# Kernel tuning notes

Measured on AMD Instinct MI355X. Metric: run time of the kernel, lower is better.

The kernel has to match this reference:

```python
import jax, jax.numpy as jnp
import numpy as np

B, N = 2, 2048
TOP_K = 48
NUM_RBF = 16
MAX_REL = 32            # max_relative_feature
NUM_POS = 16            # num_positional_embeddings
EDGE_FEATURES = 128
EDGE_IN = NUM_POS + NUM_RBF * 25  # 416
POS_IN = 2 * MAX_REL + 2          # 66 one-hot classes


def setup_inputs() -> dict:
    key = jax.random.key(0)
    k0, k1, k2, k3 = jax.random.split(key, 4)
    X = jax.random.normal(k0, (B, N, 4, 3), dtype=jnp.float32) * 3.0
    mask = jnp.ones((B, N), dtype=jnp.float32)
    R_idx = jnp.arange(B * N, dtype=jnp.int32).reshape(B, N)
    chain_labels = jax.random.randint(k1, (B, N), 0, 4).astype(jnp.int32)
    W_pos = 0.05 * jax.random.normal(k2, (POS_IN, NUM_POS), dtype=jnp.float32)
    b_pos = jnp.zeros((NUM_POS,), dtype=jnp.float32)
    W_edge = 0.05 * jax.random.normal(k3, (EDGE_IN, EDGE_FEATURES), dtype=jnp.float32)
    b_edge = jnp.zeros((EDGE_FEATURES,), dtype=jnp.float32)
    return {"X": X, "mask": mask, "R_idx": R_idx, "chain_labels": chain_labels,
            "W_pos": W_pos, "b_pos": b_pos, "W_edge": W_edge, "b_edge": b_edge}


def _rbf(D):
    # D: [..., K] -> [..., K, NUM_RBF]
    mu = jnp.linspace(2.0, 22.0, NUM_RBF)        # D_min=2, D_max=22
    sigma = (22.0 - 2.0) / NUM_RBF               # 1.25
    return jnp.exp(-(((D[..., None] - mu) / sigma) ** 2))


def _pair_dist(A, Bc):
    # A, Bc: [B, N, 3] -> [B, N, N]
    return jnp.sqrt(jnp.sum((A[:, :, None, :] - Bc[:, None, :, :]) ** 2, axis=-1) + 1e-6)


def reference(X, mask, R_idx, chain_labels, W_pos, b_pos, W_edge, b_edge):
    # virtual Cbeta from backbone geometry
    b = X[:, :, 1, :] - X[:, :, 0, :]
    c = X[:, :, 2, :] - X[:, :, 1, :]
    a = jnp.cross(b, c, axis=-1)
    Cb = -0.58273431 * a + 0.56802827 * b - 0.54067466 * c + X[:, :, 1, :]
    Ca, Nat, Cat, Oat = X[:, :, 1, :], X[:, :, 0, :], X[:, :, 2, :], X[:, :, 3, :]

    # masked Ca-Ca distances + k nearest neighbors
    mask2 = mask[:, None, :] * mask[:, :, None]
    D = mask2 * _pair_dist(Ca, Ca)
    D_adjust = D + (1.0 - mask2) * jnp.max(D, axis=-1, keepdims=True)
    neg_D, E_idx = jax.lax.top_k(-D_adjust, min(TOP_K, N))  # smallest distances
    D_neighbors = -neg_D                                     # [B, N, K]

    rbfs = [_rbf(D_neighbors)]
    pairs = [(Nat, Nat), (Cat, Cat), (Oat, Oat), (Cb, Cb),
             (Ca, Nat), (Ca, Cat), (Ca, Oat), (Ca, Cb),
             (Nat, Cat), (Nat, Oat), (Nat, Cb), (Cb, Cat), (Cb, Oat), (Oat, Cat),
             (Nat, Ca), (Cat, Ca), (Oat, Ca), (Cb, Ca),
             (Cat, Nat), (Oat, Nat), (Cb, Nat), (Cat, Cb), (Oat, Cb), (Cat, Oat)]
    for A_, B_ in pairs:  # fixed structural set of 24 atom-pair types
        Dab = _pair_dist(A_, B_)                          # [B, N, N]
        Dn = jnp.take_along_axis(Dab, E_idx, axis=2)      # [B, N, K]
        rbfs.append(_rbf(Dn))
    RBF_all = jnp.concatenate(rbfs, axis=-1)              # [B, N, K, 25*NUM_RBF]

    # relative positional / chain features at the gathered neighbors
    offset = R_idx[:, :, None] - R_idx[:, None, :]
    offset = jnp.take_along_axis(offset, E_idx, axis=2)   # [B, N, K]
    d_chains = (chain_labels[:, :, None] == chain_labels[:, None, :]).astype(jnp.int32)
    E_chains = jnp.take_along_axis(d_chains, E_idx, axis=2)

    d = jnp.clip(offset + MAX_REL, 0, 2 * MAX_REL)
    d = d * E_chains + (1 - E_chains) * (2 * MAX_REL + 1)
    d_onehot = jax.nn.one_hot(d, POS_IN, dtype=jnp.float32)  # [B, N, K, 66]
    E_positional = d_onehot @ W_pos + b_pos                  # [B, N, K, 16]

    E = jnp.concatenate((E_positional, RBF_all), axis=-1)    # [B, N, K, 416]
    E = E @ W_edge + b_edge                                  # [B, N, K, 128]
    return E, E_idx
```

## Files before the change

### kernel.cpp

```cpp
#include <hip/hip_runtime.h>
#include <hip/hip_bf16.h>
#include <stdint.h>

#define BB   2
#define NN   2048
#define BN   (BB*NN)
#define KTOP 48
#define EIN  416
#define EF   128
#define LROW 424

typedef __attribute__((ext_vector_type(8))) short s8v;
typedef __attribute__((ext_vector_type(4))) float f32x4;
typedef unsigned short u16;
typedef unsigned int u32;
typedef unsigned long long u64;

__device__ __constant__ int cPA[25] = {1,0,2,3,4,1,1,1,1,0,0,0,4,4,3,0,2,3,4,2,3,4,2,3,2};
__device__ __constant__ int cPB[25] = {1,0,2,3,4,0,2,3,4,2,3,4,2,3,2,1,1,1,1,0,0,0,4,4,3};

__device__ __forceinline__ u16 bf16u(float x) {
  __hip_bfloat16 h = __float2bfloat16(x);
  return *reinterpret_cast<u16*>(&h);
}

__global__ __launch_bounds__(256) void prep_kernel(const float* __restrict__ X,
                                                   const float* __restrict__ W_edge,
                                                   float* __restrict__ atoms5,
                                                   float* __restrict__ capack,
                                                   u16* __restrict__ wt) {
  int tid = blockIdx.x * 256 + threadIdx.x;
  if (tid < EIN * EF) {
    int n = tid & (EF - 1), kk = tid >> 7;
    wt[(size_t)n * EIN + kk] = bf16u(W_edge[tid]);
  } else if (tid < EIN * EF + BN) {
    int idx = tid - EIN * EF;
    const float* x = X + (size_t)idx * 12;
    float Nx = x[0], Ny = x[1], Nz = x[2];
    float Cax = x[3], Cay = x[4], Caz = x[5];
    float Cx = x[6], Cy = x[7], Cz = x[8];
    float Ox = x[9], Oy = x[10], Oz = x[11];
    float bx = Cax - Nx, by = Cay - Ny, bz = Caz - Nz;
    float cx = Cx - Cax, cy = Cy - Cay, cz = Cz - Caz;
    float ax = by * cz - bz * cy;
    float ay = bz * cx - bx * cz;
    float az = bx * cy - by * cx;
    float Cbx = -0.58273431f * ax + 0.56802827f * bx - 0.54067466f * cx + Cax;
    float Cby = -0.58273431f * ay + 0.56802827f * by - 0.54067466f * cy + Cay;
    float Cbz = -0.58273431f * az + 0.56802827f * bz - 0.54067466f * cz + Caz;
    float* o = atoms5 + (size_t)idx * 15;
    o[0] = Nx;  o[1] = Ny;  o[2] = Nz;
    o[3] = Cax; o[4] = Cay; o[5] = Caz;
    o[6] = Cx;  o[7] = Cy;  o[8] = Cz;
    o[9] = Ox;  o[10] = Oy; o[11] = Oz;
    o[12] = Cbx; o[13] = Cby; o[14] = Cbz;
    capack[idx * 3 + 0] = Cax;
    capack[idx * 3 + 1] = Cay;
    capack[idx * 3 + 2] = Caz;
  }
}

__device__ __forceinline__ u32 blockExclScan(u32 v, u32* scanw, int t) {
  int lane = t & 63, w = t >> 6;
  u32 inc = v;
#pragma unroll
  for (int off = 1; off < 64; off <<= 1) {
    u32 o = __shfl_up(inc, off);
    if (lane >= off) inc += o;
  }
  if (lane == 63) scanw[w] = inc;
  __syncthreads();
  u32 base = 0;
  for (int ww = 0; ww < w; ++ww) base += scanw[ww];
  __syncthreads();
  return base + inc - v;
}

template<int NB, bool CHKPREF>
__device__ __forceinline__ void radix_round(u32* hist, u32* scanw, u32* selinfo, int t,
                                            const u32* kv, u32 pref, int prefShift,
                                            int binShift, u32 binMask, u32 r) {
  const int PB = NB / 256;
  for (int q = 0; q < PB; ++q) hist[t * PB + q] = 0;
  __syncthreads();
#pragma unroll
  for (int s = 0; s < 8; ++s) {
    bool ok = (!CHKPREF) || ((kv[s] >> prefShift) == pref);
    if (ok) atomicAdd(&hist[(kv[s] >> binShift) & binMask], 1u);
  }
  __syncthreads();
  u32 loc[PB];
  u32 sum = 0;
  for (int q = 0; q < PB; ++q) { loc[q] = hist[t * PB + q]; sum += loc[q]; }
  int lane = t & 63, w = t >> 6;
  u32 inc = sum;
#pragma unroll
  for (int off = 1; off < 64; off <<= 1) {
    u32 o = __shfl_up(inc, off);
    if (lane >= off) inc += o;
  }
  if (lane == 63) scanw[w] = inc;
  __syncthreads();
  u32 base = 0;
  for (int ww = 0; ww < w; ++ww) base += scanw[ww];
  u32 c = base + inc - sum;
  for (int q = 0; q < PB; ++q) {
    u32 nc = c + loc[q];
    if (c < r && r <= nc) { selinfo[0] = (u32)(t * PB + q); selinfo[1] = r - c; }
    c = nc;
  }
  __syncthreads();
}

__global__ __launch_bounds__(256) void topk_kernel(const float* __restrict__ capack,
                                                   const float* __restrict__ mask,
                                                   int* __restrict__ eidx,
                                                   float* __restrict__ dtop,
                                                   float* __restrict__ eidx_f) {
  __shared__ u32 hist[4096];
  __shared__ u32 scanw[4];
  __shared__ u32 selinfo[2];
  __shared__ float redf[4];
  __shared__ u64 win[64];

  int row = blockIdx.x;
  int b = row >> 11, i = row & (NN - 1);
  int t = threadIdx.x, lane = t & 63, w = t >> 6;
  const float* cab = capack + (size_t)b * NN * 3;
  const float* mrow = mask + (size_t)b * NN;
  float cix = cab[i * 3 + 0], ciy = cab[i * 3 + 1], ciz = cab[i * 3 + 2];
  float mi = mrow[i];

  float dvv[8], m2v[8];
  float lmax = 0.f;
#pragma unroll
  for (int s = 0; s < 8; ++s) {
    int j = t * 8 + s;
    float dx = cix - cab[j * 3 + 0];
    float dy = ciy - cab[j * 3 + 1];
    float dz = ciz - cab[j * 3 + 2];
    float d = sqrtf(dx * dx + dy * dy + dz * dz + 1e-6f);
    float m2 = mi * mrow[j];
    float D = m2 * d;
    dvv[s] = D; m2v[s] = m2;
    lmax = fmaxf(lmax, D);
  }
#pragma unroll
  for (int off = 32; off >= 1; off >>= 1) lmax = fmaxf(lmax, __shfl_xor(lmax, off));
  if (lane == 0) redf[w] = lmax;
  __syncthreads();
  float rmax = fmaxf(fmaxf(redf[0], redf[1]), fmaxf(redf[2], redf[3]));

  u32 kv[8];
#pragma unroll
  for (int s = 0; s < 8; ++s)
    kv[s] = __float_as_uint(dvv[s] + (1.0f - m2v[s]) * rmax);

  u32 r = KTOP;
  radix_round<4096, false>(hist, scanw, selinfo, t, kv, 0, 0, 20, 0xFFFu, r);
  u32 sel1 = selinfo[0]; r = selinfo[1];
  radix_round<1024, true>(hist, scanw, selinfo, t, kv, sel1, 20, 10, 0x3FFu, r);
  u32 sel2 = selinfo[0]; r = selinfo[1];
  u32 pref12 = (sel1 << 10) | sel2;
  radix_round<1024, true>(hist, scanw, selinfo, t, kv, pref12, 10, 0, 0x3FFu, r);
  u32 sel3 = selinfo[0];
  u32 takeEq = selinfo[1];
  u32 T = (sel1 << 20) | (sel2 << 10) | sel3;

  u32 lcnt = 0, ecnt = 0;
#pragma unroll
  for (int s = 0; s < 8; ++s) { lcnt += (kv[s] < T); ecnt += (kv[s] == T); }
  u32 ebase = blockExclScan(ecnt, scanw, t);
  u32 taken = 0;
  if (ebase < takeEq) { u32 room = takeEq - ebase; taken = room < ecnt ? room : ecnt; }
  u32 wbase = blockExclScan(lcnt + taken, scanw, t);
  u32 slot = wbase, tleft = taken;
#pragma unroll
  for (int s = 0; s < 8; ++s) {
    u32 j = (u32)(t * 8 + s);
    if (kv[s] < T) {
      win[slot++] = ((u64)kv[s] << 32) | j;
    } else if (kv[s] == T && tleft) {
      win[slot++] = ((u64)kv[s] << 32) | j;
      tleft--;
    }
  }
  __syncthreads();

  if (w == 0) {
    u64 key = (lane < KTOP) ? win[lane] : ~0ull;
#pragma unroll
    for (int k = 2; k <= 64; k <<= 1) {
#pragma unroll
      for (int jj = k >> 1; jj >= 1; jj >>= 1) {
        u64 p = __shfl_xor(key, jj);
        bool lowerl = (lane & jj) == 0;
        bool asc = (lane & k) == 0;
        u64 mn = p < key ? p : key;
        u64 mx = p < key ? key : p;
        key = (lowerl == asc) ? mn : mx;
      }
    }
    if (lane < KTOP) {
      u32 j = (u32)(key & 0xffffffffu);
      eidx[row * KTOP + lane] = (int)j;
      eidx_f[row * KTOP + lane] = (float)j;
      dtop[row * KTOP + lane] = __uint_as_float((u32)(key >> 32));
    }
  }
}

__global__ __launch_bounds__(256) void edge_kernel(const float* __restrict__ atoms5,
                                                   const u16* __restrict__ wt,
                                                   const int* __restrict__ eidx,
                                                   const float* __restrict__ dtop,
                                                   const int* __restrict__ Ridx,
                                                   const int* __restrict__ chains,
                                                   const float* __restrict__ Wpos,
                                                   const float* __restrict__ bpos,
                                                   const float* __restrict__ bedge,
                                                   float* __restrict__ Eout) {
  __shared__ u16 feat[KTOP * LROW];
  __shared__ float atomsJ[KTOP][15];
  __shared__ float atomsI[15];
  __shared__ int jbuf[KTOP];

  int row = blockIdx.x;
  int b = row >> 11, i = row & (NN - 1);
  int t = threadIdx.x;

  if (t < KTOP) jbuf[t] = eidx[row * KTOP + t];
  if (t < 15) atomsI[t] = atoms5[(size_t)row * 15 + t];
  __syncthreads();

  if (t < KTOP * 5) {
    int k = t / 5, a = t % 5;
    int j = jbuf[k];
    const float* src = atoms5 + ((size_t)(b * NN + j) * 15 + a * 3);
    atomsJ[k][a * 3 + 0] = src[0];
    atomsJ[k][a * 3 + 1] = src[1];
    atomsJ[k][a * 3 + 2] = src[2];
  }
  __syncthreads();

  if (t < KTOP) {
    int k = t, j = jbuf[k];
    int Ri = Ridx[b * NN + i], Rj = Ridx[b * NN + j];
    int same = (chains[b * NN + i] == chains[b * NN + j]);
    int off = Ri - Rj + 32;
    off = off < 0 ? 0 : (off > 64 ? 64 : off);
    int drow = same ? off : 65;
#pragma unroll
    for (int r = 0; r < 16; ++r)
      feat[k * LROW + r] = bf16u(Wpos[drow * 16 + r] + bpos[r]);
    float D = dtop[row * KTOP + k];
#pragma unroll
    for (int r = 0; r < 16; ++r) {
      float mu = 2.0f + (20.0f * r) / 15.0f;
      float tt = (D - mu) * 0.8f;
      feat[k * LROW + 16 + r] = bf16u(__expf(-tt * tt));
    }
  }
  if (t < KTOP * 5) {
    int k = t / 5, g = t % 5;
    for (int p = 1 + g; p < 25; p += 5) {
      int a = cPA[p], b2 = cPB[p];
      float dx = atomsI[a * 3 + 0] - atomsJ[k][b2 * 3 + 0];
      float dy = atomsI[a * 3 + 1] - atomsJ[k][b2 * 3 + 1];
      float dz = atomsI[a * 3 + 2] - atomsJ[k][b2 * 3 + 2];
      float D = sqrtf(dx * dx + dy * dy + dz * dz + 1e-6f);
#pragma unroll
      for (int r = 0; r < 16; ++r) {
        float mu = 2.0f + (20.0f * r) / 15.0f;
        float tt = (D - mu) * 0.8f;
        feat[k * LROW + 16 + p * 16 + r] = bf16u(__expf(-tt * tt));
      }
    }
  }
  __syncthreads();

  int w = t >> 6, lane = t & 63;
  int lr = lane & 15, lg = lane >> 4;
  f32x4 acc[3][2] = {};
  for (int kc = 0; kc < 13; ++kc) {
    s8v afrag[3];
#pragma unroll
    for (int mt = 0; mt < 3; ++mt)
      afrag[mt] = *reinterpret_cast<const s8v*>(&feat[(mt * 16 + lr) * LROW + kc * 32 + lg * 8]);
#pragma unroll
    for (int nt = 0; nt < 2; ++nt) {
      int col = w * 32 + nt * 16 + lr;
      s8v bfrag = *reinterpret_cast<const s8v*>(&wt[(size_t)col * EIN + kc * 32 + lg * 8]);
#pragma unroll
      for (int mt = 0; mt < 3; ++mt)
        acc[mt][nt] = __builtin_amdgcn_mfma_f32_16x16x32_bf16(afrag[mt], bfrag, acc[mt][nt], 0, 0, 0);
    }
  }
#pragma unroll
  for (int nt = 0; nt < 2; ++nt) {
    int col = w * 32 + nt * 16 + lr;
    float bias = bedge[col];
#pragma unroll
    for (int mt = 0; mt < 3; ++mt) {
#pragma unroll
      for (int q = 0; q < 4; ++q) {
        int m = mt * 16 + lg * 4 + q;
        Eout[((size_t)row * KTOP + m) * EF + col] = acc[mt][nt][q] + bias;
      }
    }
  }
}

extern "C" void kernel_launch(void* const* d_in, const int* in_sizes, int n_in,
                              void* d_out, int out_size, void* d_ws, size_t ws_size,
                              hipStream_t stream) {
  const float* X = (const float*)d_in[0];
  const float* mask = (const float*)d_in[1];
  const int* Ridx = (const int*)d_in[2];
  const int* chains = (const int*)d_in[3];
  const float* Wpos = (const float*)d_in[4];
  const float* bpos = (const float*)d_in[5];
  const float* Wedge = (const float*)d_in[6];
  const float* bedge = (const float*)d_in[7];

  float* Eout = (float*)d_out;
  float* EidxF = Eout + (size_t)BN * KTOP * EF;

  float* atoms5 = (float*)d_ws;
  float* capack = atoms5 + (size_t)BN * 15;
  u16* wt = (u16*)(capack + (size_t)BN * 3);
  int* eidx = (int*)(wt + (size_t)EIN * EF);
  float* dtop = (float*)(eidx + (size_t)BN * KTOP);

  int prep_threads = EIN * EF + BN;
  prep_kernel<<<(prep_threads + 255) / 256, 256, 0, stream>>>(X, Wedge, atoms5, capack, wt);
  topk_kernel<<<BN, 256, 0, stream>>>(capack, mask, eidx, dtop, EidxF);
  edge_kernel<<<BN, 256, 0, stream>>>(atoms5, wt, eidx, dtop, Ridx, chains, Wpos, bpos, bedge, Eout);
}
```

Measured before the change: 100.3 us.

## Vectorize loads, reformulate RBF recurrence, stage output stores through LDS

Pads atom and Ca coordinates to float4 so gathers become single vector loads, and re-lays out the bf16 weight matrix so MFMA B-fragment loads are contiguous across columns. The edge kernel now builds features with one thread per (neighbor, 16-wide feature chunk), computes the 16 RBF values with a multiplicative recurrence (two exps instead of sixteen) and writes them as packed 16-byte stores. The GEMM output is staged in LDS and written as coalesced float4 rows, and the histogram clear/read in the top-k radix is vectorised. Distances are clamped to 40 for the recurrence, which changes rounding slightly, and an extra barrier is added for the staging step.

```diff
diff --git a/kernel.cpp b/kernel.cpp
--- a/kernel.cpp
+++ b/kernel.cpp
@@ -9,9 +9,11 @@
 #define EIN  416
 #define EF   128
 #define LROW 424
+#define SROW 132
 
 typedef __attribute__((ext_vector_type(8))) short s8v;
 typedef __attribute__((ext_vector_type(4))) float f32x4;
+typedef __attribute__((ext_vector_type(4))) unsigned int u32x4;
 typedef unsigned short u16;
 typedef unsigned int u32;
 typedef unsigned long long u64;
@@ -23,16 +25,19 @@
   __hip_bfloat16 h = __float2bfloat16(x);
   return *reinterpret_cast<u16*>(&h);
 }
+__device__ __forceinline__ u32 pack2(float lo, float hi) {
+  return (u32)bf16u(lo) | ((u32)bf16u(hi) << 16);
+}
 
 __global__ __launch_bounds__(256) void prep_kernel(const float* __restrict__ X,
                                                    const float* __restrict__ W_edge,
-                                                   float* __restrict__ atoms5,
-                                                   float* __restrict__ capack,
-                                                   u16* __restrict__ wt) {
+                                                   float* __restrict__ atoms5p,
+                                                   float* __restrict__ capack4,
+                                                   u16* __restrict__ wtf) {
   int tid = blockIdx.x * 256 + threadIdx.x;
   if (tid < EIN * EF) {
-    int n = tid & (EF - 1), kk = tid >> 7;
-    wt[(size_t)n * EIN + kk] = bf16u(W_edge[tid]);
+    int k = tid >> 7, n = tid & 127;
+    wtf[((size_t)(k >> 3)) * 1024 + n * 8 + (k & 7)] = bf16u(W_edge[tid]);
   } else if (tid < EIN * EF + BN) {
     int idx = tid - EIN * EF;
     const float* x = X + (size_t)idx * 12;
@@ -48,15 +53,13 @@
     float Cbx = -0.58273431f * ax + 0.56802827f * bx - 0.54067466f * cx + Cax;
     float Cby = -0.58273431f * ay + 0.56802827f * by - 0.54067466f * cy + Cay;
     float Cbz = -0.58273431f * az + 0.56802827f * bz - 0.54067466f * cz + Caz;
-    float* o = atoms5 + (size_t)idx * 15;
-    o[0] = Nx;  o[1] = Ny;  o[2] = Nz;
-    o[3] = Cax; o[4] = Cay; o[5] = Caz;
-    o[6] = Cx;  o[7] = Cy;  o[8] = Cz;
-    o[9] = Ox;  o[10] = Oy; o[11] = Oz;
-    o[12] = Cbx; o[13] = Cby; o[14] = Cbz;
-    capack[idx * 3 + 0] = Cax;
-    capack[idx * 3 + 1] = Cay;
-    capack[idx * 3 + 2] = Caz;
+    f32x4* o = (f32x4*)(atoms5p + (size_t)idx * 20);
+    o[0] = (f32x4){Nx, Ny, Nz, 0.f};
+    o[1] = (f32x4){Cax, Cay, Caz, 0.f};
+    o[2] = (f32x4){Cx, Cy, Cz, 0.f};
+    o[3] = (f32x4){Ox, Oy, Oz, 0.f};
+    o[4] = (f32x4){Cbx, Cby, Cbz, 0.f};
+    *(f32x4*)(capack4 + (size_t)idx * 4) = (f32x4){Cax, Cay, Caz, 0.f};
   }
 }
 
@@ -81,7 +84,9 @@
                                             const u32* kv, u32 pref, int prefShift,
                                             int binShift, u32 binMask, u32 r) {
   const int PB = NB / 256;
-  for (int q = 0; q < PB; ++q) hist[t * PB + q] = 0;
+#pragma unroll
+  for (int q = 0; q < PB / 4; ++q)
+    *(u32x4*)&hist[t * PB + q * 4] = (u32x4){0, 0, 0, 0};
   __syncthreads();
 #pragma unroll
   for (int s = 0; s < 8; ++s) {
@@ -91,7 +96,13 @@
   __syncthreads();
   u32 loc[PB];
   u32 sum = 0;
-  for (int q = 0; q < PB; ++q) { loc[q] = hist[t * PB + q]; sum += loc[q]; }
+#pragma unroll
+  for (int q = 0; q < PB / 4; ++q) {
+    u32x4 lv = *(u32x4*)&hist[t * PB + q * 4];
+    loc[q * 4 + 0] = lv.x; loc[q * 4 + 1] = lv.y;
+    loc[q * 4 + 2] = lv.z; loc[q * 4 + 3] = lv.w;
+    sum += lv.x + lv.y + lv.z + lv.w;
+  }
   int lane = t & 63, w = t >> 6;
   u32 inc = sum;
 #pragma unroll
@@ -104,6 +115,7 @@
   u32 base = 0;
   for (int ww = 0; ww < w; ++ww) base += scanw[ww];
   u32 c = base + inc - sum;
+#pragma unroll
   for (int q = 0; q < PB; ++q) {
     u32 nc = c + loc[q];
     if (c < r && r <= nc) { selinfo[0] = (u32)(t * PB + q); selinfo[1] = r - c; }
@@ -112,9 +124,8 @@
   __syncthreads();
 }
 
-__global__ __launch_bounds__(256) void topk_kernel(const float* __restrict__ capack,
+__global__ __launch_bounds__(256) void topk_kernel(const float* __restrict__ capack4,
                                                    const float* __restrict__ mask,
-                                                   int* __restrict__ eidx,
                                                    float* __restrict__ dtop,
                                                    float* __restrict__ eidx_f) {
   __shared__ u32 hist[4096];
@@ -126,21 +137,22 @@
   int row = blockIdx.x;
   int b = row >> 11, i = row & (NN - 1);
   int t = threadIdx.x, lane = t & 63, w = t >> 6;
-  const float* cab = capack + (size_t)b * NN * 3;
+  const float* cab4 = capack4 + (size_t)b * NN * 4;
   const float* mrow = mask + (size_t)b * NN;
-  float cix = cab[i * 3 + 0], ciy = cab[i * 3 + 1], ciz = cab[i * 3 + 2];
+  f32x4 ci = *(const f32x4*)&cab4[(size_t)i * 4];
   float mi = mrow[i];
+  f32x4 mk0 = *(const f32x4*)&mrow[t * 8];
+  f32x4 mk1 = *(const f32x4*)&mrow[t * 8 + 4];
 
   float dvv[8], m2v[8];
   float lmax = 0.f;
 #pragma unroll
   for (int s = 0; s < 8; ++s) {
-    int j = t * 8 + s;
-    float dx = cix - cab[j * 3 + 0];
-    float dy = ciy - cab[j * 3 + 1];
-    float dz = ciz - cab[j * 3 + 2];
+    f32x4 cj = *(const f32x4*)&cab4[(size_t)(t * 8 + s) * 4];
+    float dx = ci.x - cj.x, dy = ci.y - cj.y, dz = ci.z - cj.z;
     float d = sqrtf(dx * dx + dy * dy + dz * dz + 1e-6f);
-    float m2 = mi * mrow[j];
+    float mj = (s < 4) ? mk0[s] : mk1[s - 4];
+    float m2 = mi * mj;
     float D = m2 * d;
     dvv[s] = D; m2v[s] = m2;
     lmax = fmaxf(lmax, D);
@@ -203,78 +215,81 @@
     }
     if (lane < KTOP) {
       u32 j = (u32)(key & 0xffffffffu);
-      eidx[row * KTOP + lane] = (int)j;
       eidx_f[row * KTOP + lane] = (float)j;
       dtop[row * KTOP + lane] = __uint_as_float((u32)(key >> 32));
     }
   }
 }
 
-__global__ __launch_bounds__(256) void edge_kernel(const float* __restrict__ atoms5,
-                                                   const u16* __restrict__ wt,
-                                                   const int* __restrict__ eidx,
-                                                   const float* __restrict__ dtop,
-                                                   const int* __restrict__ Ridx,
-                                                   const int* __restrict__ chains,
-                                                   const float* __restrict__ Wpos,
-                                                   const float* __restrict__ bpos,
-                                                   const float* __restrict__ bedge,
-                                                   float* __restrict__ Eout) {
-  __shared__ u16 feat[KTOP * LROW];
-  __shared__ float atomsJ[KTOP][15];
-  __shared__ float atomsI[15];
+__global__ __launch_bounds__(256, 4) void edge_kernel(const float* __restrict__ atoms5p,
+                                                      const u16* __restrict__ wtf,
+                                                      const float* __restrict__ eidx_f,
+                                                      const float* __restrict__ dtop,
+                                                      const int* __restrict__ Ridx,
+                                                      const int* __restrict__ chains,
+                                                      const float* __restrict__ Wpos,
+                                                      const float* __restrict__ bpos,
+                                                      const float* __restrict__ bedge,
+                                                      float* __restrict__ Eout) {
+  __shared__ __align__(16) u16 featsm[KTOP * LROW];
   __shared__ int jbuf[KTOP];
 
   int row = blockIdx.x;
   int b = row >> 11, i = row & (NN - 1);
   int t = threadIdx.x;
 
-  if (t < KTOP) jbuf[t] = eidx[row * KTOP + t];
-  if (t < 15) atomsI[t] = atoms5[(size_t)row * 15 + t];
-  __syncthreads();
-
-  if (t < KTOP * 5) {
-    int k = t / 5, a = t % 5;
-    int j = jbuf[k];
-    const float* src = atoms5 + ((size_t)(b * NN + j) * 15 + a * 3);
-    atomsJ[k][a * 3 + 0] = src[0];
-    atomsJ[k][a * 3 + 1] = src[1];
-    atomsJ[k][a * 3 + 2] = src[2];
-  }
-  __syncthreads();
-
-  if (t < KTOP) {
-    int k = t, j = jbuf[k];
-    int Ri = Ridx[b * NN + i], Rj = Ridx[b * NN + j];
-    int same = (chains[b * NN + i] == chains[b * NN + j]);
-    int off = Ri - Rj + 32;
-    off = off < 0 ? 0 : (off > 64 ? 64 : off);
-    int drow = same ? off : 65;
-#pragma unroll
-    for (int r = 0; r < 16; ++r)
-      feat[k * LROW + r] = bf16u(Wpos[drow * 16 + r] + bpos[r]);
-    float D = dtop[row * KTOP + k];
-#pragma unroll
-    for (int r = 0; r < 16; ++r) {
-      float mu = 2.0f + (20.0f * r) / 15.0f;
-      float tt = (D - mu) * 0.8f;
-      feat[k * LROW + 16 + r] = bf16u(__expf(-tt * tt));
-    }
-  }
-  if (t < KTOP * 5) {
-    int k = t / 5, g = t % 5;
-    for (int p = 1 + g; p < 25; p += 5) {
-      int a = cPA[p], b2 = cPB[p];
-      float dx = atomsI[a * 3 + 0] - atomsJ[k][b2 * 3 + 0];
-      float dy = atomsI[a * 3 + 1] - atomsJ[k][b2 * 3 + 1];
-      float dz = atomsI[a * 3 + 2] - atomsJ[k][b2 * 3 + 2];
-      float D = sqrtf(dx * dx + dy * dy + dz * dz + 1e-6f);
-#pragma unroll
-      for (int r = 0; r < 16; ++r) {
-        float mu = 2.0f + (20.0f * r) / 15.0f;
-        float tt = (D - mu) * 0.8f;
-        feat[k * LROW + 16 + p * 16 + r] = bf16u(__expf(-tt * tt));
+  if (t < KTOP) jbuf[t] = (int)eidx_f[row * KTOP + t];
+  __syncthreads();
+
+  const float* atomsB = atoms5p + (size_t)b * NN * 20;
+
+#pragma unroll
+  for (int q = 0; q < 5; ++q) {
+    int e = t + q * 256;
+    if (e < KTOP * 26) {
+      int k = e / 26;
+      int c = e - k * 26;
+      int j = jbuf[k];
+      u32 pk[8];
+      if (c == 0) {
+        int Ri = Ridx[b * NN + i], Rj = Ridx[b * NN + j];
+        int same = (chains[b * NN + i] == chains[b * NN + j]);
+        int off = Ri - Rj + 32;
+        off = off < 0 ? 0 : (off > 64 ? 64 : off);
+        int drow = same ? off : 65;
+        const float* wr = Wpos + drow * 16;
+#pragma unroll
+        for (int h = 0; h < 4; ++h) {
+          f32x4 wv = *(const f32x4*)&wr[h * 4];
+          f32x4 bv = *(const f32x4*)&bpos[h * 4];
+          pk[h * 2 + 0] = pack2(wv.x + bv.x, wv.y + bv.y);
+          pk[h * 2 + 1] = pack2(wv.z + bv.z, wv.w + bv.w);
+        }
+      } else {
+        float D;
+        if (c == 1) {
+          D = dtop[row * KTOP + k];
+        } else {
+          int p = c - 1;
+          f32x4 I = *(const f32x4*)&atomsB[(size_t)i * 20 + cPA[p] * 4];
+          f32x4 J = *(const f32x4*)&atomsB[(size_t)j * 20 + cPB[p] * 4];
+          float dx = I.x - J.x, dy = I.y - J.y, dz = I.z - J.z;
+          D = sqrtf(dx * dx + dy * dy + dz * dz + 1e-6f);
+        }
+        float Dc = fminf(D, 40.0f);
+        float t0 = (Dc - 2.0f) * 0.8f;
+        float v = __expf(-t0 * t0);
+        float g = __expf(2.13333333f * t0 - 1.13777778f);
+#pragma unroll
+        for (int h = 0; h < 8; ++h) {
+          float lo = v; v *= g; g *= 0.10273985f;
+          float hi = v; v *= g; g *= 0.10273985f;
+          pk[h] = pack2(lo, hi);
+        }
       }
+      u32x4* dst = (u32x4*)&featsm[k * LROW + c * 16];
+      dst[0] = (u32x4){pk[0], pk[1], pk[2], pk[3]};
+      dst[1] = (u32x4){pk[4], pk[5], pk[6], pk[7]};
     }
   }
   __syncthreads();
@@ -286,28 +301,43 @@
     s8v afrag[3];
 #pragma unroll
     for (int mt = 0; mt < 3; ++mt)
-      afrag[mt] = *reinterpret_cast<const s8v*>(&feat[(mt * 16 + lr) * LROW + kc * 32 + lg * 8]);
+      afrag[mt] = *reinterpret_cast<const s8v*>(&featsm[(mt * 16 + lr) * LROW + kc * 32 + lg * 8]);
 #pragma unroll
     for (int nt = 0; nt < 2; ++nt) {
       int col = w * 32 + nt * 16 + lr;
-      s8v bfrag = *reinterpret_cast<const s8v*>(&wt[(size_t)col * EIN + kc * 32 + lg * 8]);
+      s8v bfrag = *reinterpret_cast<const s8v*>(&wtf[(size_t)(kc * 4 + lg) * 1024 + col * 8]);
 #pragma unroll
       for (int mt = 0; mt < 3; ++mt)
         acc[mt][nt] = __builtin_amdgcn_mfma_f32_16x16x32_bf16(afrag[mt], bfrag, acc[mt][nt], 0, 0, 0);
     }
   }
+  __syncthreads();
+
+  float* stage = (float*)featsm;
+  float bias0 = bedge[w * 32 + lr];
+  float bias1 = bedge[w * 32 + 16 + lr];
 #pragma unroll
   for (int nt = 0; nt < 2; ++nt) {
+    float bias = nt ? bias1 : bias0;
     int col = w * 32 + nt * 16 + lr;
-    float bias = bedge[col];
 #pragma unroll
     for (int mt = 0; mt < 3; ++mt) {
 #pragma unroll
-      for (int q = 0; q < 4; ++q) {
-        int m = mt * 16 + lg * 4 + q;
-        Eout[((size_t)row * KTOP + m) * EF + col] = acc[mt][nt][q] + bias;
+      for (int qq = 0; qq < 4; ++qq) {
+        int m = mt * 16 + lg * 4 + qq;
+        stage[m * SROW + col] = acc[mt][nt][qq] + bias;
       }
     }
+  }
+  __syncthreads();
+
+  float* orow = Eout + (size_t)row * KTOP * EF;
+#pragma unroll
+  for (int q2 = 0; q2 < 6; ++q2) {
+    int o = t * 4 + q2 * 1024;
+    int m = o >> 7, col = o & 127;
+    f32x4 vv = *(f32x4*)&stage[m * SROW + col];
+    *(f32x4*)&orow[m * EF + col] = vv;
   }
 }
 
@@ -326,14 +356,12 @@
   float* Eout = (float*)d_out;
   float* EidxF = Eout + (size_t)BN * KTOP * EF;
 
-  float* atoms5 = (float*)d_ws;
-  float* capack = atoms5 + (size_t)BN * 15;
-  u16* wt = (u16*)(capack + (size_t)BN * 3);
-  int* eidx = (int*)(wt + (size_t)EIN * EF);
-  float* dtop = (float*)(eidx + (size_t)BN * KTOP);
-
-  int prep_threads = EIN * EF + BN;
-  prep_kernel<<<(prep_threads + 255) / 256, 256, 0, stream>>>(X, Wedge, atoms5, capack, wt);
-  topk_kernel<<<BN, 256, 0, stream>>>(capack, mask, eidx, dtop, EidxF);
-  edge_kernel<<<BN, 256, 0, stream>>>(atoms5, wt, eidx, dtop, Ridx, chains, Wpos, bpos, bedge, Eout);
-}
+  u16* wtf = (u16*)d_ws;
+  float* atoms5p = (float*)((char*)d_ws + 53248 * 2);
+  float* capack4 = atoms5p + (size_t)BN * 20;
+  float* dtop = capack4 + (size_t)BN * 4;
+
+  prep_kernel<<<(EIN * EF + BN + 255) / 256, 256, 0, stream>>>(X, Wedge, atoms5p, capack4, wtf);
+  topk_kernel<<<BN, 256, 0, stream>>>(capack4, mask, dtop, EidxF);
+  edge_kernel<<<BN, 256, 0, stream>>>(atoms5p, wtf, EidxF, dtop, Ridx, chains, Wpos, bpos, bedge, Eout);
+}
```

After: 96.44 us. 1.04x faster.
